# Kernel tuning notes

Measured on AMD Instinct MI355X. Metric: run time of the kernel, lower is better.

## Reference

```python
import jax, jax.numpy as jnp
import numpy as np

EPS = 1e-7

def fake_quant(x, bits):
    """Per-tensor affine fake-quantization (dnn-gating TorchRoundToBits),
    matching torch.fake_quantize_per_tensor_affine with dynamic range."""
    fp_max = jax.lax.stop_gradient(jnp.max(x))
    fp_min = jax.lax.stop_gradient(jnp.min(x))
    qmax = float(2 ** bits - 1)
    qmin = 0.0
    scale = (fp_max - fp_min) / (qmax - qmin) + EPS
    zero_point = jnp.trunc(qmin - fp_min / scale)  # int() cast in torch truncates
    q = jnp.round(x / scale + zero_point)
    qc = jnp.clip(q, qmin, qmax)
    return (qc - zero_point) * scale

def conv2d(x, w, stride=1, padding=1):
    return jax.lax.conv_general_dilated(
        x, w,
        window_strides=(stride, stride),
        padding=[(padding, padding), (padding, padding)],
        dimension_numbers=('NCHW', 'OIHW', 'NCHW'))

def setup_inputs() -> dict:
    key = jax.random.key(0)
    k1, k2 = jax.random.split(key)
    x = jax.random.normal(k1, (32, 256, 56, 56), dtype=jnp.float32)
    # kaiming-like init for a 3x3 conv with 256 in-channels
    fan_in = 256 * 3 * 3
    weight = jax.random.normal(k2, (256, 256, 3, 3), dtype=jnp.float32) / np.sqrt(fan_in)
    return {"x": x, "weight": weight}

def reference(x, weight):
    WBITS, ABITS, PGABITS = 8, 8, 4
    TH = 0.99
    w_q = fake_quant(weight, WBITS)          # quantized weights (shared by both convs)
    msb_in = fake_quant(x, PGABITS)          # low-precision (MSB) input
    msb_out = conv2d(msb_in, w_q)            # [32,256,56,56] prediction pass
    lsb_in = fake_quant(x, ABITS) - msb_in   # residual (LSB) input
    lsb_out = conv2d(lsb_in, w_q)            # high-precision correction pass
    mask = (jax.nn.sigmoid(msb_out) > TH).astype(msb_out.dtype)
    return msb_out + mask * lsb_out
```

## Files before the change

kernel.cpp:

```cpp
#include <hip/hip_runtime.h>
#include <stdint.h>
#include <stddef.h>

typedef int v4i  __attribute__((ext_vector_type(4)));
typedef int v16i __attribute__((ext_vector_type(16)));

struct QParams {
  float s4, z4, s8, z8, sw, zw;
  float s4sw, s8sw;
  int dw;
};

__device__ __forceinline__ unsigned enc_f(float f) {
  unsigned u = __float_as_uint(f);
  return (u & 0x80000000u) ? ~u : (u | 0x80000000u);
}
__device__ __forceinline__ float dec_f(unsigned e) {
  unsigned u = (e & 0x80000000u) ? (e ^ 0x80000000u) : ~e;
  return __uint_as_float(u);
}

__global__ void k_init(unsigned* mm, unsigned* zp) {
  int t = threadIdx.x;
  if (t < 128) zp[t] = 0u;
  if (t == 0) { mm[0] = 0xFFFFFFFFu; mm[1] = 0u; mm[2] = 0xFFFFFFFFu; mm[3] = 0u; }
}

__global__ void k_minmax2(const float4* __restrict__ x, int nx4,
                          const float4* __restrict__ w, int nw4, unsigned* mm) {
  const float4* p; int n4; unsigned* slot; int base; int nblk;
  if (blockIdx.x < 1024) { p = x; n4 = nx4; slot = mm;     base = blockIdx.x;        nblk = 1024; }
  else                   { p = w; n4 = nw4; slot = mm + 2; base = blockIdx.x - 1024; nblk = 64; }
  float lmin = 3.4e38f, lmax = -3.4e38f;
  for (int i = base * blockDim.x + threadIdx.x; i < n4; i += nblk * blockDim.x) {
    float4 v = p[i];
    lmin = fminf(lmin, fminf(fminf(v.x, v.y), fminf(v.z, v.w)));
    lmax = fmaxf(lmax, fmaxf(fmaxf(v.x, v.y), fmaxf(v.z, v.w)));
  }
  for (int off = 32; off; off >>= 1) {
    lmin = fminf(lmin, __shfl_down(lmin, off, 64));
    lmax = fmaxf(lmax, __shfl_down(lmax, off, 64));
  }
  __shared__ float smin[4], smax[4];
  int w2 = threadIdx.x >> 6, lane = threadIdx.x & 63;
  if (lane == 0) { smin[w2] = lmin; smax[w2] = lmax; }
  __syncthreads();
  if (threadIdx.x == 0) {
    float a = fminf(fminf(smin[0], smin[1]), fminf(smin[2], smin[3]));
    float b = fmaxf(fmaxf(smax[0], smax[1]), fmaxf(smax[2], smax[3]));
    atomicMin(&slot[0], enc_f(a));
    atomicMax(&slot[1], enc_f(b));
  }
}

__global__ void k_params(const unsigned* mm, QParams* q) {
  float xmin = dec_f(mm[0]), xmax = dec_f(mm[1]);
  float wmin = dec_f(mm[2]), wmax = dec_f(mm[3]);
  float s4 = (xmax - xmin) / 15.0f + 1e-7f;
  float z4 = truncf(0.0f - xmin / s4);
  float s8 = (xmax - xmin) / 255.0f + 1e-7f;
  float z8 = truncf(0.0f - xmin / s8);
  float sw = (wmax - wmin) / 255.0f + 1e-7f;
  float zw = truncf(0.0f - wmin / sw);
  q->s4 = s4; q->z4 = z4; q->s8 = s8; q->z8 = z8; q->sw = sw; q->zw = zw;
  q->s4sw = s4 * sw; q->s8sw = s8 * sw;
  q->dw = 128 - (int)zw;
}

__global__ void k_quant_w(const float* __restrict__ w, const QParams* __restrict__ q,
                          char* __restrict__ Wc) {
  __shared__ char sm[2304];
  int b = blockIdx.x;
  int tid = threadIdx.x;
  float sw = q->sw, zw = q->zw;
  const float* src = w + (size_t)b * 2304;
#pragma unroll
  for (int j = 0; j < 9; ++j) {
    int o = j * 256 + tid;
    float qf = rintf(__fdiv_rn(src[o], sw) + zw);
    qf = fminf(fmaxf(qf, 0.0f), 255.0f);
    int c = o / 9, jj = o - c * 9;
    sm[jj * 256 + c] = (char)((int)qf - 128);
  }
  __syncthreads();
  if (tid < 64) {
#pragma unroll
    for (int j = 0; j < 9; ++j)
      *(unsigned*)(Wc + (size_t)j * 65536 + b * 256 + tid * 4) =
          *(const unsigned*)(sm + j * 256 + tid * 4);
  }
}

__device__ __forceinline__ void quant2(float v, float s4, float z4, float s8, float z8,
                                       char& o4, char& o8) {
  float q4 = rintf(__fdiv_rn(v, s4) + z4);
  q4 = fminf(fmaxf(q4, 0.0f), 15.0f);
  o4 = (char)(int)(q4 - z4);
  float q8 = rintf(__fdiv_rn(v, s8) + z8);
  q8 = fminf(fmaxf(q8, 0.0f), 255.0f);
  int t8 = (int)(q8 - z8);
  o8 = (char)max(-128, min(127, t8));
}

__global__ void k_quant_x(const float4* __restrict__ x4, const QParams* __restrict__ q,
                          char* __restrict__ A4, char* __restrict__ A8,
                          int* __restrict__ CS4, int* __restrict__ CS8) {
  __shared__ char sm4[56 * 260];
  __shared__ char sm8[56 * 260];
  __shared__ int cp4[56][4], cp8[56][4];
  int bx = blockIdx.x;
  int n = bx / 56, y = bx % 56;
  int tid = threadIdx.x;
  float s4 = q->s4, z4 = q->z4, s8 = q->s8, z8 = q->z8;
  const float4* xrow = x4 + (size_t)n * 200704 + y * 14;
#pragma unroll 2
  for (int it = 0; it < 14; ++it) {
    int idx = it * 256 + tid;
    int c = idx / 14, xq = idx - c * 14;
    float4 v = xrow[(size_t)c * 784 + xq];
    int b = (xq * 4) * 260 + c;
    char a0, b0; quant2(v.x, s4, z4, s8, z8, a0, b0);
    char a1, b1; quant2(v.y, s4, z4, s8, z8, a1, b1);
    char a2, b2; quant2(v.z, s4, z4, s8, z8, a2, b2);
    char a3, b3; quant2(v.w, s4, z4, s8, z8, a3, b3);
    sm4[b] = a0; sm4[b + 260] = a1; sm4[b + 520] = a2; sm4[b + 780] = a3;
    sm8[b] = b0; sm8[b + 260] = b1; sm8[b + 520] = b2; sm8[b + 780] = b3;
  }
  __syncthreads();
  if (tid < 224) {
    int xc = tid >> 2, qq = tid & 3;
    const unsigned* r4 = (const unsigned*)(sm4 + xc * 260 + qq * 64);
    const unsigned* r8 = (const unsigned*)(sm8 + xc * 260 + qq * 64);
    int a = 0, b = 0;
#pragma unroll
    for (int cw = 0; cw < 16; ++cw) {
      unsigned u = r4[cw], v = r8[cw];
      a += (int)(signed char)(u) + (int)(signed char)(u >> 8)
         + (int)(signed char)(u >> 16) + (int)(signed char)(u >> 24);
      b += (int)(signed char)(v) + (int)(signed char)(v >> 8)
         + (int)(signed char)(v >> 16) + (int)(signed char)(v >> 24);
    }
    cp4[xc][qq] = a; cp8[xc][qq] = b;
  }
  __syncthreads();
  int pixbase = n * 3136 + y * 56;
  if (tid < 56) {
    CS4[pixbase + tid] = cp4[tid][0] + cp4[tid][1] + cp4[tid][2] + cp4[tid][3];
    CS8[pixbase + tid] = cp8[tid][0] + cp8[tid][1] + cp8[tid][2] + cp8[tid][3];
  }
  unsigned* A4w = (unsigned*)A4;
  unsigned* A8w = (unsigned*)A8;
#pragma unroll 2
  for (int it = 0; it < 14; ++it) {
    int idx = it * 256 + tid;
    int xc = idx >> 6, wd = idx & 63;
    size_t o = (size_t)(pixbase + xc) * 64 + wd;
    A4w[o] = *(const unsigned*)(sm4 + xc * 260 + wd * 4);
    A8w[o] = *(const unsigned*)(sm8 + xc * 260 + wd * 4);
  }
}

__global__ void k_wsum(const int* __restrict__ CS4, const int* __restrict__ CS8,
                       int* __restrict__ S4, int* __restrict__ S8) {
  int p = blockIdx.x * 256 + threadIdx.x;
  if (p >= 100352) return;
  int rem = p % 3136;
  int y = rem / 56, xc = rem % 56;
  int a = 0, b = 0;
#pragma unroll
  for (int dy = -1; dy <= 1; ++dy) {
    if ((unsigned)(y + dy) >= 56u) continue;
#pragma unroll
    for (int dx = -1; dx <= 1; ++dx) {
      if ((unsigned)(xc + dx) >= 56u) continue;
      int qq = p + dy * 56 + dx;
      a += CS4[qq]; b += CS8[qq];
    }
  }
  S4[p] = a; S8[p] = b;
}

#define GLD16(gp, lp)                                                         \
  __builtin_amdgcn_global_load_lds((const __attribute__((address_space(1))) void*)(gp), \
                                   (__attribute__((address_space(3))) void*)(lp), 16, 0, 0)

__device__ __forceinline__ float pg_merge(int a4v, int a8v, float fs4, float fs8) {
  float msb = fs4 * (float)a4v;
  float c8  = fs8 * (float)a8v;
  float lsb = c8 - msb;
  float sig = 1.0f / (1.0f + expf(-msb));
  return msb + (sig > 0.99f ? lsb : 0.0f);
}

struct StagePtrs {
  const char* aBase0; const char* aBase1;
  const char* a8Base0; const char* a8Base1;
  const char* bBase0; const char* bBase1;
  const char* zp0;
  unsigned vm0, vm1;
};

__device__ __forceinline__ void issue_half(int s, int half, const StagePtrs& P,
                                           char* dA4, char* dA8, char* dB) {
  int win = s >> 2;
  int cs = (s & 3) << 6;
  int dy = win / 3 - 1;
  int dx = win - (dy + 1) * 3 - 1;
  int doff = (dy * 56 + dx) * 256 + cs;
  bool ok0 = (P.vm0 >> win) & 1;
  bool ok1 = (P.vm1 >> win) & 1;
  if (half == 0) {
    const char* g40 = ok0 ? P.aBase0 + doff : P.zp0;
    const char* g41 = ok1 ? P.aBase1 + doff : P.zp0;
    const char* gB0 = P.bBase0 + win * 65536 + cs;
    if (s >= 36) gB0 = P.zp0;
    GLD16(g40, dA4); GLD16(g41, dA4 + 1024); GLD16(gB0, dB);
  } else {
    const char* g80 = ok0 ? P.a8Base0 + doff : P.zp0;
    const char* g81 = ok1 ? P.a8Base1 + doff : P.zp0;
    const char* gB1 = P.bBase1 + win * 65536 + cs;
    if (s >= 36) gB1 = P.zp0;
    GLD16(g80, dA8); GLD16(g81, dA8 + 1024); GLD16(gB1, dB + 1024);
  }
}

__global__ __launch_bounds__(256, 2) void k_conv(
    const char* __restrict__ A4, const char* __restrict__ A8,
    const char* __restrict__ Wc,
    const int* __restrict__ S4, const int* __restrict__ S8,
    const QParams* __restrict__ q, const char* __restrict__ zpage,
    float* __restrict__ out) {
  __shared__ char smA4[3][8192], smA8[3][8192], smB[3][8192];
  const size_t ASZ = 25690112;
  int tid = threadIdx.x;
  int w = tid >> 6, lane = tid & 63;

  int bid = blockIdx.x;
  int swz = (bid & 7) * 196 + (bid >> 3);
  int m0 = (swz >> 1) * 128;
  int n0 = (swz & 1) * 128;
  int wm = w >> 1, wn = w & 1;

  int chunk = lane & 3;
  int r0 = (w << 5) + (lane >> 2);
  int r1 = r0 + 16;
  int cg0 = chunk ^ ((r0 >> 1) & 3);
  int cg1 = chunk ^ ((r1 >> 1) & 3);
  int p0 = m0 + r0, p1 = m0 + r1;
  int rem0 = p0 % 3136, rem1 = p1 % 3136;
  int y0 = rem0 / 56, x0 = rem0 % 56;
  int y1 = rem1 / 56, x1 = rem1 % 56;

  StagePtrs P;
  P.aBase0 = A4 + (size_t)p0 * 256 + cg0 * 16;
  P.aBase1 = A4 + (size_t)p1 * 256 + cg1 * 16;
  P.a8Base0 = P.aBase0 + ASZ;
  P.a8Base1 = P.aBase1 + ASZ;
  P.bBase0 = Wc + (n0 + r0) * 256 + cg0 * 16;
  P.bBase1 = Wc + (n0 + r1) * 256 + cg1 * 16;
  P.zp0 = zpage + chunk * 16;
  P.vm0 = 0; P.vm1 = 0;
#pragma unroll
  for (int win = 0; win < 9; ++win) {
    int dy = win / 3 - 1, dx = win % 3 - 1;
    P.vm0 |= (unsigned)(((unsigned)(y0 + dy) < 56u) & ((unsigned)(x0 + dx) < 56u)) << win;
    P.vm1 |= (unsigned)(((unsigned)(y1 + dy) < 56u) & ((unsigned)(x1 + dx) < 56u)) << win;
  }

  char* dA4 = &smA4[0][w << 11];
  char* dA8 = &smA8[0][w << 11];
  char* dB  = &smB[0][w << 11];
  const char* smA4f = &smA4[0][0];
  const char* smA8f = &smA8[0][0];
  const char* smBf  = &smB[0][0];

  v16i acc4[2][2] = {}, acc8[2][2] = {};
  int r31 = lane & 31, qh = lane >> 5;

  int offA[2][2], offB[2][2];
#pragma unroll
  for (int fm = 0; fm < 2; ++fm) {
    int row = wm * 64 + fm * 32 + r31;
    int swl = (row >> 1) & 3;
#pragma unroll
    for (int kc = 0; kc < 2; ++kc)
      offA[fm][kc] = row * 64 + (((kc * 2 + qh) ^ swl) << 4);
  }
#pragma unroll
  for (int fn = 0; fn < 2; ++fn) {
    int row = wn * 64 + fn * 32 + r31;
    int swl = (row >> 1) & 3;
#pragma unroll
    for (int kc = 0; kc < 2; ++kc)
      offB[fn][kc] = row * 64 + (((kc * 2 + qh) ^ swl) << 4);
  }

#define SUBPHASE(S, RB, WB, KC)                                               \
  {                                                                           \
    v4i a4f[2], a8f[2], bf[2];                                                \
    _Pragma("unroll")                                                         \
    for (int fm = 0; fm < 2; ++fm) {                                          \
      a4f[fm] = *(const v4i*)(smA4f + (RB) * 8192 + offA[fm][KC]);            \
      a8f[fm] = *(const v4i*)(smA8f + (RB) * 8192 + offA[fm][KC]);            \
    }                                                                         \
    _Pragma("unroll")                                                         \
    for (int fn = 0; fn < 2; ++fn)                                            \
      bf[fn] = *(const v4i*)(smBf + (RB) * 8192 + offB[fn][KC]);              \
    issue_half((S) + 2, KC, P, dA4 + (WB) * 8192, dA8 + (WB) * 8192,          \
               dB + (WB) * 8192);                                             \
    asm volatile("s_barrier" ::: "memory");                                   \
    asm volatile("s_waitcnt lgkmcnt(0)" ::: "memory");                        \
    __builtin_amdgcn_s_setprio(1);                                            \
    _Pragma("unroll")                                                         \
    for (int fm = 0; fm < 2; ++fm)                                            \
      _Pragma("unroll")                                                       \
      for (int fn = 0; fn < 2; ++fn) {                                        \
        acc4[fm][fn] = __builtin_amdgcn_mfma_i32_32x32x32_i8(a4f[fm], bf[fn], acc4[fm][fn], 0, 0, 0); \
        acc8[fm][fn] = __builtin_amdgcn_mfma_i32_32x32x32_i8(a8f[fm], bf[fn], acc8[fm][fn], 0, 0, 0); \
      }                                                                       \
    __builtin_amdgcn_s_setprio(0);                                            \
  }

#define PHASE(S, RB, WB)                                                      \
  {                                                                           \
    asm volatile("s_waitcnt vmcnt(6)" ::: "memory");                          \
    asm volatile("s_barrier" ::: "memory");                                   \
    SUBPHASE(S, RB, WB, 0)                                                    \
    SUBPHASE(S, RB, WB, 1)                                                    \
  }

  issue_half(0, 0, P, dA4, dA8, dB);
  issue_half(0, 1, P, dA4, dA8, dB);
  issue_half(1, 0, P, dA4 + 8192, dA8 + 8192, dB + 8192);
  issue_half(1, 1, P, dA4 + 8192, dA8 + 8192, dB + 8192);

#pragma unroll 1
  for (int sp = 0; sp < 12; ++sp) {
    int s0 = sp * 3;
    PHASE(s0,     0, 2);
    PHASE(s0 + 1, 1, 0);
    PHASE(s0 + 2, 2, 1);
  }
  asm volatile("s_waitcnt vmcnt(0)" ::: "memory");
#undef PHASE
#undef SUBPHASE

  float fs4 = q->s4sw, fs8 = q->s8sw;
  int dwv = q->dw;
#pragma unroll
  for (int fm = 0; fm < 2; ++fm)
#pragma unroll
    for (int fn = 0; fn < 2; ++fn) {
      int kout = n0 + wn * 64 + fn * 32 + r31;
      int pb = m0 + wm * 64 + fm * 32 + 4 * qh;
#pragma unroll
      for (int rg = 0; rg < 4; ++rg) {
        int pr = pb + 8 * rg;
        int4 sv4 = *(const int4*)(S4 + pr);
        int4 sv8 = *(const int4*)(S8 + pr);
        float4 res;
        res.x = pg_merge(acc4[fm][fn][rg * 4 + 0] + dwv * sv4.x,
                         acc8[fm][fn][rg * 4 + 0] + dwv * sv8.x, fs4, fs8);
        res.y = pg_merge(acc4[fm][fn][rg * 4 + 1] + dwv * sv4.y,
                         acc8[fm][fn][rg * 4 + 1] + dwv * sv8.y, fs4, fs8);
        res.z = pg_merge(acc4[fm][fn][rg * 4 + 2] + dwv * sv4.z,
                         acc8[fm][fn][rg * 4 + 2] + dwv * sv8.z, fs4, fs8);
        res.w = pg_merge(acc4[fm][fn][rg * 4 + 3] + dwv * sv4.w,
                         acc8[fm][fn][rg * 4 + 3] + dwv * sv8.w, fs4, fs8);
        int nimg = pr / 3136;
        int rem = pr - nimg * 3136;
        *(float4*)(out + (size_t)nimg * 802816 + (size_t)kout * 3136 + rem) = res;
      }
    }
}

extern "C" void kernel_launch(void* const* d_in, const int* in_sizes, int n_in,
                              void* d_out, int out_size, void* d_ws, size_t ws_size,
                              hipStream_t stream) {
  const float* x  = (const float*)d_in[0];
  const float* wt = (const float*)d_in[1];
  float* out = (float*)d_out;

  char* ws = (char*)d_ws;
  unsigned* mm = (unsigned*)ws;
  QParams* prm = (QParams*)(ws + 64);
  char* zpage = ws + 256;
  char* A4 = ws + 1024;
  const size_t ASZ = 25690112;
  char* A8 = A4 + ASZ;
  int* CS4 = (int*)(A8 + ASZ);
  int* CS8 = CS4 + 100352;
  int* S4  = CS8 + 100352;
  int* S8  = S4 + 100352;
  char* Wc = (char*)(S8 + 100352);

  k_init<<<1, 256, 0, stream>>>(mm, (unsigned*)zpage);
  k_minmax2<<<1088, 256, 0, stream>>>((const float4*)x, 25690112 / 4,
                                      (const float4*)wt, 589824 / 4, mm);
  k_params<<<1, 1, 0, stream>>>(mm, prm);
  k_quant_w<<<256, 256, 0, stream>>>(wt, prm, Wc);
  k_quant_x<<<1792, 256, 0, stream>>>((const float4*)x, prm, A4, A8, CS4, CS8);
  k_wsum<<<392, 256, 0, stream>>>(CS4, CS8, S4, S8);
  k_conv<<<dim3(1568), 256, 0, stream>>>(A4, A8, Wc, S4, S8, prm, zpage, out);
}
```

Measured before the change: 408.4 us.

## Replace atomic min/max with per-block partials and fuse param/quant kernels

Each min/max block now writes its partial (min,max) pair to its own slot instead of using global atomics, which removes the init kernel. Every block of a merged quantization kernel re-reduces the partials and computes the quantization parameters in shared memory. This folds k_init, k_params, k_quant_w and k_quant_x into one launch, cutting three kernel launches and their serialization gaps. In exchange, the small reduction is repeated redundantly in all 2048 blocks.

Result: faster. 374.3 us (-8.3%).

```diff
diff --git a/kernel.cpp b/kernel.cpp
--- a/kernel.cpp
+++ b/kernel.cpp
@@ -11,26 +11,12 @@
   int dw;
 };
 
-__device__ __forceinline__ unsigned enc_f(float f) {
-  unsigned u = __float_as_uint(f);
-  return (u & 0x80000000u) ? ~u : (u | 0x80000000u);
-}
-__device__ __forceinline__ float dec_f(unsigned e) {
-  unsigned u = (e & 0x80000000u) ? (e ^ 0x80000000u) : ~e;
-  return __uint_as_float(u);
-}
-
-__global__ void k_init(unsigned* mm, unsigned* zp) {
-  int t = threadIdx.x;
-  if (t < 128) zp[t] = 0u;
-  if (t == 0) { mm[0] = 0xFFFFFFFFu; mm[1] = 0u; mm[2] = 0xFFFFFFFFu; mm[3] = 0u; }
-}
-
 __global__ void k_minmax2(const float4* __restrict__ x, int nx4,
-                          const float4* __restrict__ w, int nw4, unsigned* mm) {
-  const float4* p; int n4; unsigned* slot; int base; int nblk;
-  if (blockIdx.x < 1024) { p = x; n4 = nx4; slot = mm;     base = blockIdx.x;        nblk = 1024; }
-  else                   { p = w; n4 = nw4; slot = mm + 2; base = blockIdx.x - 1024; nblk = 64; }
+                          const float4* __restrict__ w, int nw4,
+                          float2* __restrict__ mmX, float2* __restrict__ mmW) {
+  const float4* p; int n4; float2* slot; int base; int nblk;
+  if (blockIdx.x < 1024) { p = x; n4 = nx4; slot = mmX + blockIdx.x;          base = blockIdx.x;        nblk = 1024; }
+  else                   { p = w; n4 = nw4; slot = mmW + (blockIdx.x - 1024); base = blockIdx.x - 1024; nblk = 64; }
   float lmin = 3.4e38f, lmax = -3.4e38f;
   for (int i = base * blockDim.x + threadIdx.x; i < n4; i += nblk * blockDim.x) {
     float4 v = p[i];
@@ -46,48 +32,10 @@
   if (lane == 0) { smin[w2] = lmin; smax[w2] = lmax; }
   __syncthreads();
   if (threadIdx.x == 0) {
-    float a = fminf(fminf(smin[0], smin[1]), fminf(smin[2], smin[3]));
-    float b = fmaxf(fmaxf(smax[0], smax[1]), fmaxf(smax[2], smax[3]));
-    atomicMin(&slot[0], enc_f(a));
-    atomicMax(&slot[1], enc_f(b));
-  }
-}
-
-__global__ void k_params(const unsigned* mm, QParams* q) {
-  float xmin = dec_f(mm[0]), xmax = dec_f(mm[1]);
-  float wmin = dec_f(mm[2]), wmax = dec_f(mm[3]);
-  float s4 = (xmax - xmin) / 15.0f + 1e-7f;
-  float z4 = truncf(0.0f - xmin / s4);
-  float s8 = (xmax - xmin) / 255.0f + 1e-7f;
-  float z8 = truncf(0.0f - xmin / s8);
-  float sw = (wmax - wmin) / 255.0f + 1e-7f;
-  float zw = truncf(0.0f - wmin / sw);
-  q->s4 = s4; q->z4 = z4; q->s8 = s8; q->z8 = z8; q->sw = sw; q->zw = zw;
-  q->s4sw = s4 * sw; q->s8sw = s8 * sw;
-  q->dw = 128 - (int)zw;
-}
-
-__global__ void k_quant_w(const float* __restrict__ w, const QParams* __restrict__ q,
-                          char* __restrict__ Wc) {
-  __shared__ char sm[2304];
-  int b = blockIdx.x;
-  int tid = threadIdx.x;
-  float sw = q->sw, zw = q->zw;
-  const float* src = w + (size_t)b * 2304;
-#pragma unroll
-  for (int j = 0; j < 9; ++j) {
-    int o = j * 256 + tid;
-    float qf = rintf(__fdiv_rn(src[o], sw) + zw);
-    qf = fminf(fmaxf(qf, 0.0f), 255.0f);
-    int c = o / 9, jj = o - c * 9;
-    sm[jj * 256 + c] = (char)((int)qf - 128);
-  }
-  __syncthreads();
-  if (tid < 64) {
-#pragma unroll
-    for (int j = 0; j < 9; ++j)
-      *(unsigned*)(Wc + (size_t)j * 65536 + b * 256 + tid * 4) =
-          *(const unsigned*)(sm + j * 256 + tid * 4);
+    float2 r;
+    r.x = fminf(fminf(smin[0], smin[1]), fminf(smin[2], smin[3]));
+    r.y = fmaxf(fmaxf(smax[0], smax[1]), fmaxf(smax[2], smax[3]));
+    *slot = r;
   }
 }
 
@@ -102,16 +50,83 @@
   o8 = (char)max(-128, min(127, t8));
 }
 
-__global__ void k_quant_x(const float4* __restrict__ x4, const QParams* __restrict__ q,
-                          char* __restrict__ A4, char* __restrict__ A8,
-                          int* __restrict__ CS4, int* __restrict__ CS8) {
+__global__ void k_quant(const float4* __restrict__ x4, const float* __restrict__ wt,
+                        const float2* __restrict__ mmX, const float2* __restrict__ mmW,
+                        char* __restrict__ A4, char* __restrict__ A8,
+                        int* __restrict__ CS4, int* __restrict__ CS8,
+                        char* __restrict__ Wc,
+                        QParams* __restrict__ prm, unsigned* __restrict__ zp) {
   __shared__ char sm4[56 * 260];
   __shared__ char sm8[56 * 260];
   __shared__ int cp4[56][4], cp8[56][4];
+  __shared__ float s_red[4][4];
+  __shared__ QParams sq;
+  int tid = threadIdx.x;
+
+  {
+    float xmn = 3.4e38f, xmx = -3.4e38f, wmn = 3.4e38f, wmx = -3.4e38f;
+#pragma unroll
+    for (int i = 0; i < 4; ++i) {
+      float2 v = mmX[i * 256 + tid];
+      xmn = fminf(xmn, v.x); xmx = fmaxf(xmx, v.y);
+    }
+    if (tid < 64) { float2 v = mmW[tid]; wmn = v.x; wmx = v.y; }
+    for (int off = 32; off; off >>= 1) {
+      xmn = fminf(xmn, __shfl_down(xmn, off, 64));
+      xmx = fmaxf(xmx, __shfl_down(xmx, off, 64));
+      wmn = fminf(wmn, __shfl_down(wmn, off, 64));
+      wmx = fmaxf(wmx, __shfl_down(wmx, off, 64));
+    }
+    int wv = tid >> 6, ln = tid & 63;
+    if (ln == 0) { s_red[wv][0] = xmn; s_red[wv][1] = xmx; s_red[wv][2] = wmn; s_red[wv][3] = wmx; }
+    __syncthreads();
+    if (tid == 0) {
+      float xmin = fminf(fminf(s_red[0][0], s_red[1][0]), fminf(s_red[2][0], s_red[3][0]));
+      float xmax = fmaxf(fmaxf(s_red[0][1], s_red[1][1]), fmaxf(s_red[2][1], s_red[3][1]));
+      float wmin = fminf(fminf(s_red[0][2], s_red[1][2]), fminf(s_red[2][2], s_red[3][2]));
+      float wmax = fmaxf(fmaxf(s_red[0][3], s_red[1][3]), fmaxf(s_red[2][3], s_red[3][3]));
+      float s4 = (xmax - xmin) / 15.0f + 1e-7f;
+      sq.s4 = s4; sq.z4 = truncf(0.0f - xmin / s4);
+      float s8 = (xmax - xmin) / 255.0f + 1e-7f;
+      sq.s8 = s8; sq.z8 = truncf(0.0f - xmin / s8);
+      float sw = (wmax - wmin) / 255.0f + 1e-7f;
+      sq.sw = sw; sq.zw = truncf(0.0f - wmin / sw);
+      sq.s4sw = s4 * sw; sq.s8sw = s8 * sw;
+      sq.dw = 128 - (int)sq.zw;
+    }
+    __syncthreads();
+  }
+
+  if (blockIdx.x >= 1792) {
+    int b = blockIdx.x - 1792;
+    float sw = sq.sw, zw = sq.zw;
+    char* smw = sm4;
+    const float* src = wt + (size_t)b * 2304;
+#pragma unroll
+    for (int j = 0; j < 9; ++j) {
+      int o = j * 256 + tid;
+      float qf = rintf(__fdiv_rn(src[o], sw) + zw);
+      qf = fminf(fmaxf(qf, 0.0f), 255.0f);
+      int c = o / 9, jj = o - c * 9;
+      smw[jj * 256 + c] = (char)((int)qf - 128);
+    }
+    __syncthreads();
+    if (tid < 64) {
+#pragma unroll
+      for (int j = 0; j < 9; ++j)
+        *(unsigned*)(Wc + (size_t)j * 65536 + b * 256 + tid * 4) =
+            *(const unsigned*)(smw + j * 256 + tid * 4);
+    }
+    if (blockIdx.x == 1792) {
+      if (tid < 128) zp[tid] = 0u;
+      if (tid == 0) *prm = sq;
+    }
+    return;
+  }
+
   int bx = blockIdx.x;
   int n = bx / 56, y = bx % 56;
-  int tid = threadIdx.x;
-  float s4 = q->s4, z4 = q->z4, s8 = q->s8, z8 = q->z8;
+  float s4 = sq.s4, z4 = sq.z4, s8 = sq.s8, z8 = sq.z8;
   const float4* xrow = x4 + (size_t)n * 200704 + y * 14;
 #pragma unroll 2
   for (int it = 0; it < 14; ++it) {
@@ -382,10 +397,11 @@
   float* out = (float*)d_out;
 
   char* ws = (char*)d_ws;
-  unsigned* mm = (unsigned*)ws;
-  QParams* prm = (QParams*)(ws + 64);
-  char* zpage = ws + 256;
-  char* A4 = ws + 1024;
+  float2* mmX = (float2*)ws;
+  float2* mmW = (float2*)(ws + 8192);
+  QParams* prm = (QParams*)(ws + 8960);
+  char* zpage = ws + 9728;
+  char* A4 = ws + 10240;
   const size_t ASZ = 25690112;
   char* A8 = A4 + ASZ;
   int* CS4 = (int*)(A8 + ASZ);
@@ -394,12 +410,10 @@
   int* S8  = S4 + 100352;
   char* Wc = (char*)(S8 + 100352);
 
-  k_init<<<1, 256, 0, stream>>>(mm, (unsigned*)zpage);
   k_minmax2<<<1088, 256, 0, stream>>>((const float4*)x, 25690112 / 4,
-                                      (const float4*)wt, 589824 / 4, mm);
-  k_params<<<1, 1, 0, stream>>>(mm, prm);
-  k_quant_w<<<256, 256, 0, stream>>>(wt, prm, Wc);
-  k_quant_x<<<1792, 256, 0, stream>>>((const float4*)x, prm, A4, A8, CS4, CS8);
+                                      (const float4*)wt, 589824 / 4, mmX, mmW);
+  k_quant<<<2048, 256, 0, stream>>>((const float4*)x, wt, mmX, mmW,
+                                    A4, A8, CS4, CS8, Wc, prm, (unsigned*)zpage);
   k_wsum<<<392, 256, 0, stream>>>(CS4, CS8, S4, S8);
   k_conv<<<dim3(1568), 256, 0, stream>>>(A4, A8, Wc, S4, S8, prm, zpage, out);
 }
```
